# Kernel tuning notes

Measured on AMD Instinct MI355X. Metric: run time of the kernel, lower is better.

## Reference

```python
import jax, jax.numpy as jnp
import numpy as np


def setup_inputs() -> dict:
    key = jax.random.key(0)
    k1, k2 = jax.random.split(key)
    B, D, H, W = 32, 64, 32, 32
    K = 1024
    z_e = jax.random.normal(k1, (B, D, H, W), dtype=jnp.float32)
    # original init: uniform(-1/K, 1/K); use same scale
    emb = jax.random.uniform(k2, (K, D), dtype=jnp.float32, minval=-1.0 / K, maxval=1.0 / K)
    return {"z_e": z_e, "emb": emb}


COMMITMENT_COST = 0.25


def reference(z_e, emb):
    # z_e: [B, D, H, W], emb: [K, D]
    B, D, H, W = z_e.shape
    K = emb.shape[0]
    z = jnp.transpose(z_e, (0, 2, 3, 1))           # [B, H, W, D]
    flat = z.reshape(-1, D)                        # [N, D]
    N = flat.shape[0]

    dist = (
        jnp.sum(flat * flat, axis=1, keepdims=True)
        + jnp.sum(emb * emb, axis=1)
        - 2.0 * flat @ emb.T
    )
    idx = jnp.argmin(dist, axis=1)                 # [N]
    encodings = jax.nn.one_hot(idx, K, dtype=flat.dtype)  # [N, K]
    z_q = (encodings @ emb).reshape(z.shape)       # [B, H, W, D]

    e_latent_loss = jnp.mean((jax.lax.stop_gradient(z_q) - z) ** 2)
    q_latent_loss = jnp.mean((z_q - jax.lax.stop_gradient(z)) ** 2)
    loss = q_latent_loss + COMMITMENT_COST * e_latent_loss

    # straight-through estimator
    z_st = z + jax.lax.stop_gradient(z_q - z)

    avg_probs = jnp.sum(encodings, axis=0) / jnp.float32(N)
    perplexity = jnp.exp(-jnp.sum(avg_probs * jnp.log(avg_probs + 1e-10)))

    return (jnp.transpose(z_st, (0, 3, 1, 2)), loss, perplexity, encodings)
```

## Files before the change

kernel.cpp:

```cpp
#include <hip/hip_runtime.h>
#include <stdint.h>
#include <math.h>

constexpr int Kk  = 1024;

constexpr int OUT0_N   = 32 * 64 * 1024;
constexpr int OUT_LOSS = OUT0_N;
constexpr int OUT_PERP = OUT0_N + 1;
constexpr int OUT_ENC  = OUT0_N + 2;

constexpr size_t WS_CNT = 0;
constexpr size_t WS_LP  = 4096;
constexpr size_t WS_BN  = 12288;
constexpr size_t WS_MBN = 16384;
constexpr size_t WS_EBF = 20480;
constexpr size_t WS_KEY = 151552;

typedef short bf16x8 __attribute__((ext_vector_type(8)));
typedef float f32x16 __attribute__((ext_vector_type(16)));

__device__ __forceinline__ float norm64v(const float4* __restrict__ p) {
#pragma clang fp contract(off)
    float tt[64];
#pragma unroll
    for (int q = 0; q < 16; ++q) {
        float4 v = p[q];
        tt[4 * q + 0] = v.x * v.x;
        tt[4 * q + 1] = v.y * v.y;
        tt[4 * q + 2] = v.z * v.z;
        tt[4 * q + 3] = v.w * v.w;
    }
    float r[8];
#pragma unroll
    for (int j = 0; j < 8; ++j) r[j] = tt[j];
#pragma unroll
    for (int i = 8; i < 64; i += 8)
#pragma unroll
        for (int j = 0; j < 8; ++j) r[j] += tt[i + j];
    return ((r[0] + r[1]) + (r[2] + r[3])) + ((r[4] + r[5]) + (r[6] + r[7]));
}

__device__ __forceinline__ uint32_t fsort(float f) {
    uint32_t b = __float_as_uint(f);
    return (b & 0x80000000u) ? ~b : (b | 0x80000000u);
}

__device__ __forceinline__ unsigned short f2bf(float f) {
    uint32_t u = __float_as_uint(f);
    uint32_t r = (u + 0x7fffu + ((u >> 16) & 1u)) >> 16;
    return (unsigned short)r;
}

__device__ __forceinline__ unsigned long long
exact_key_bn(float A, const float* __restrict__ xr, const float* __restrict__ emb,
             const float* __restrict__ Bn_g, uint32_t code) {
    const float4* e4 = (const float4*)(emb + (size_t)code * 64);
    float4 ev[16];
#pragma unroll
    for (int q = 0; q < 16; ++q) ev[q] = e4[q];
    float C = 0.f;
#pragma unroll
    for (int q = 0; q < 16; ++q) {
        C = __builtin_fmaf(xr[4 * q + 0], ev[q].x, C);
        C = __builtin_fmaf(xr[4 * q + 1], ev[q].y, C);
        C = __builtin_fmaf(xr[4 * q + 2], ev[q].z, C);
        C = __builtin_fmaf(xr[4 * q + 3], ev[q].w, C);
    }
    float s = A + Bn_g[code];
    float dist = __builtin_fmaf(-2.f, C, s);
    return ((unsigned long long)fsort(dist) << 32) | code;
}

__global__ __launch_bounds__(256)
void norms_kernel(const float* __restrict__ emb, float* __restrict__ Bn_g,
                  float* __restrict__ maxbn, uint32_t* __restrict__ counts,
                  unsigned char* __restrict__ ebf16g) {
    __shared__ float wred[4];
    const int t = threadIdx.x, lane = t & 63, wv = t >> 6;
    const int code = blockIdx.x * 256 + t;
    float nn = norm64v((const float4*)(emb + (size_t)code * 64));
    Bn_g[code] = nn;
    if (blockIdx.x == 0) ((uint4*)counts)[t] = make_uint4(0u, 0u, 0u, 0u);

    {
        unsigned char* base = ebf16g + (size_t)(code >> 7) * 16384 + (size_t)(code & 127) * 128;
        const int swz = (code & 7) << 4;
        const float4* e4 = (const float4*)(emb + (size_t)code * 64);
#pragma unroll
        for (int q = 0; q < 16; ++q) {
            float4 v = e4[q];
            ushort4 bv;
            bv.x = f2bf(v.x); bv.y = f2bf(v.y); bv.z = f2bf(v.z); bv.w = f2bf(v.w);
            *(ushort4*)(base + ((q * 8) ^ swz)) = bv;
        }
    }
    float mx = nn;
#pragma unroll
    for (int m = 1; m < 64; m <<= 1) mx = fmaxf(mx, __shfl_xor(mx, m, 64));
    if (lane == 0) wred[wv] = mx;
    __syncthreads();
    if (t == 0)   maxbn[blockIdx.x * 2 + 0] = fmaxf(wred[0], wred[1]);
    if (t == 128) maxbn[blockIdx.x * 2 + 1] = fmaxf(wred[2], wred[3]);
}

__global__ __launch_bounds__(256, 5)
void dist_mfma(const float* __restrict__ z_e,
               const unsigned char* __restrict__ ebf16g,
               const float* __restrict__ Bn_g, const float* __restrict__ maxbn,
               unsigned long long* __restrict__ lockey, float* __restrict__ out) {
    __shared__ unsigned short ebf[128 * 64];
    __shared__ float Bn_s[128];
    const int t = threadIdx.x, lane = t & 63, wv = t >> 6, g = lane >> 5;
    const int rg = blockIdx.x >> 3, cg = blockIdx.x & 7;
    const int n0 = rg * 128, b = n0 >> 10, hw0 = n0 & 1023;
    const float* zb = z_e + (size_t)b * 65536 + hw0;

    {
        const float4* ep = (const float4*)(ebf16g + (size_t)cg * 16384);
#pragma unroll
        for (int it = 0; it < 4; ++it) {
            float4 v = ep[it * 256 + t];
            *(float4*)((char*)ebf + (size_t)(it * 256 + t) * 16) = v;
        }
    }
    if (t < 128) Bn_s[t] = Bn_g[cg * 128 + t];

    const int rowl = wv * 32 + (lane & 31);
    float xsq = 0.f;
    bf16x8 bfr[4];
#pragma unroll
    for (int s = 0; s < 4; ++s) {
        bf16x8 f;
#pragma unroll
        for (int e = 0; e < 8; ++e) {
            int d = s * 16 + g * 8 + e;
            float x = zb[(size_t)d * 1024 + rowl];
            xsq = __builtin_fmaf(x, x, xsq);
            f[e] = (short)f2bf(x);
        }
        bfr[s] = f;
    }
    xsq += __shfl_xor(xsq, 32, 64);
    const float margin = 0.017f * sqrtf(xsq * maxbn[cg]) + 1.0e-4f;
    __syncthreads();

    const int swz = (lane & 7) << 4;
    const char* ebase = (const char*)ebf + (lane & 31) * 128;

    float4* encz = (float4*)(out + OUT_ENC) + (size_t)blockIdx.x * 4096;
    const float4 zero4 = make_float4(0.f, 0.f, 0.f, 0.f);

    float runmin = 3.4e38f;
#pragma unroll 1
    for (int tm = 0; tm < 4; ++tm) {
        encz[(size_t)(tm * 2 + 0) * 256 + t] = zero4;
        encz[(size_t)(tm * 2 + 1) * 256 + t] = zero4;
        const char* p = ebase + tm * 4096;
        f32x16 acc = {};
#pragma unroll
        for (int s = 0; s < 4; ++s)
            acc = __builtin_amdgcn_mfma_f32_32x32x16_bf16(
                *(const bf16x8*)(p + ((s * 32 + g * 16) ^ swz)), bfr[s], acc, 0, 0, 0);
#pragma unroll
        for (int r = 0; r < 16; ++r) {
            int cl = tm * 32 + (r & 3) + 8 * (r >> 2) + 4 * g;
            runmin = fminf(runmin, __builtin_fmaf(-2.f, acc[r], Bn_s[cl]));
        }
    }
    runmin = fminf(runmin, __shfl_xor(runmin, 32, 64));
    const float thr = runmin + margin;

    uint32_t cnt = 0, c0 = 0, c1 = 0, c2 = 0;
#pragma unroll 1
    for (int tm = 0; tm < 4; ++tm) {
        encz[(size_t)(8 + tm * 2 + 0) * 256 + t] = zero4;
        encz[(size_t)(8 + tm * 2 + 1) * 256 + t] = zero4;
        const char* p = ebase + tm * 4096;
        f32x16 acc = {};
#pragma unroll
        for (int s = 0; s < 4; ++s)
            acc = __builtin_amdgcn_mfma_f32_32x32x16_bf16(
                *(const bf16x8*)(p + ((s * 32 + g * 16) ^ swz)), bfr[s], acc, 0, 0, 0);
#pragma unroll
        for (int r = 0; r < 16; ++r) {
            int cl = tm * 32 + (r & 3) + 8 * (r >> 2) + 4 * g;
            float sv = __builtin_fmaf(-2.f, acc[r], Bn_s[cl]);
            if (sv <= thr) {
                uint32_t gc = (uint32_t)(cg * 128 + cl);
                if (cnt == 0u) c0 = gc; else if (cnt == 1u) c1 = gc; else if (cnt == 2u) c2 = gc;
                ++cnt;
            }
        }
    }
    uint32_t pc = __shfl_xor(cnt, 32, 64);
    uint32_t p0 = __shfl_xor(c0, 32, 64);
    uint32_t p1 = __shfl_xor(c1, 32, 64);
    uint32_t p2 = __shfl_xor(c2, 32, 64);
    if (lane < 32) {
        uint32_t tot = cnt + pc;
        uint32_t lo;
        if (tot > 3u || tot == 0u) {
            lo = 3u << 30;
        } else {
            uint32_t a0 = c0, a1 = c1, a2 = c2;
            if (cnt == 0u)      { a0 = p0; a1 = p1; a2 = p2; }
            else if (cnt == 1u) { a1 = p0; a2 = p1; }
            else if (cnt == 2u) { a2 = p0; }
            if (tot < 2u) a1 = 0u;
            if (tot < 3u) a2 = 0u;
            lo = ((tot - 1u) << 30) | (a0 & 1023u) | ((a1 & 1023u) << 10) | ((a2 & 1023u) << 20);
        }
        unsigned long long key = ((unsigned long long)__float_as_uint(runmin) << 32) | lo;
        lockey[(size_t)(n0 + rowl) * 8 + cg] = key;
    }
}

__global__ __launch_bounds__(256)
void finish_kernel(const float* __restrict__ z_e, const float* __restrict__ emb,
                   const unsigned long long* __restrict__ lockey,
                   const float* __restrict__ Bn_g,
                   const float* __restrict__ maxbn,
                   uint32_t* __restrict__ counts, double* __restrict__ lp,
                   float* __restrict__ out) {
    __shared__ float zs[32 * 68];
    __shared__ float arow[32];
    __shared__ uint32_t scode[32];
    __shared__ uint8_t ncarr[32];
    __shared__ uint8_t ovfm[32];
    __shared__ uint8_t ovfnc[32];
    __shared__ unsigned long long pkey[32][6];
    __shared__ unsigned long long okey[32];
    __shared__ uint32_t pairbuf[192];
    __shared__ uint32_t ovfbuf[32];
    __shared__ uint32_t npairs, novf;
    __shared__ float mbg_s;
    __shared__ unsigned long long rbuf[4];
    __shared__ double lred[4];
    const int t = threadIdx.x, lane = t & 63, wv = t >> 6;
    const int n0 = blockIdx.x * 32;
    const int b = n0 >> 10, hw0 = n0 & 1023;
    const int hwi = t & 31, dg = t >> 5;
    const size_t base = (size_t)b * 65536 + (size_t)(dg * 8) * 1024 + hw0 + hwi;

    if (t == 0) {
        npairs = 0u; novf = 0u;
        float mb = maxbn[0];
#pragma unroll
        for (int i = 1; i < 8; ++i) mb = fmaxf(mb, maxbn[i]);
        mbg_s = mb;
    }

    float zreg[8];
#pragma unroll
    for (int k = 0; k < 8; ++k) zreg[k] = z_e[base + (size_t)k * 1024];
#pragma unroll
    for (int m = 0; m < 2; ++m)
        *(float4*)&zs[hwi * 68 + dg * 8 + 4 * m] =
            make_float4(zreg[4 * m], zreg[4 * m + 1], zreg[4 * m + 2], zreg[4 * m + 3]);
    __syncthreads();

    if (t < 32) {
        const unsigned long long* k8 = lockey + (size_t)(n0 + t) * 8;
        unsigned long long kws[8];
#pragma unroll
        for (int i = 0; i < 8; ++i) kws[i] = k8[i];
        float gmin = 3.4e38f;
#pragma unroll
        for (int i = 0; i < 8; ++i)
            gmin = fminf(gmin, __uint_as_float((uint32_t)(kws[i] >> 32)));
        float A = norm64v((const float4*)&zs[t * 68]);
        arow[t] = A;
        const float thr = gmin + 0.017f * sqrtf(A * mbg_s) + 1.0e-4f;

        int nc = 0; uint32_t cand[6]; uint32_t om = 0;
#pragma unroll
        for (int i = 0; i < 8; ++i) {
            float f = __uint_as_float((uint32_t)(kws[i] >> 32));
            if (f > thr) continue;
            uint32_t lo = (uint32_t)kws[i], cc = lo >> 30;
            if (cc == 3u) { om |= (1u << i); }
            else {
#pragma unroll
                for (uint32_t q = 0; q < 3u; ++q)
                    if (q <= cc) {
                        if (nc < 6) cand[nc] = (lo >> (10u * q)) & 1023u;
                        ++nc;
                    }
            }
        }
        if (nc > 6 || (nc == 0 && om == 0u)) {
            ncarr[t] = 255u;
            ovfbuf[atomicAdd(&novf, 1u)] = (uint32_t)t;
        } else if (om) {
            ncarr[t] = 0u;
            ovfm[t] = (uint8_t)om;
            ovfnc[t] = (uint8_t)nc;
            ovfbuf[atomicAdd(&novf, 1u)] = (uint32_t)t;
            if (nc > 0) {
                uint32_t bs = atomicAdd(&npairs, (uint32_t)nc);
#pragma unroll
                for (int q = 0; q < 6; ++q)
                    if (q < nc)
                        pairbuf[bs + q] = ((uint32_t)t << 13) | ((uint32_t)q << 10) | cand[q];
            }
        } else if (nc == 1) {
            ncarr[t] = 1u;
            scode[t] = cand[0];
        } else {
            ncarr[t] = (uint8_t)nc;
            uint32_t bs = atomicAdd(&npairs, (uint32_t)nc);
#pragma unroll
            for (int q = 0; q < 6; ++q)
                if (q < nc)
                    pairbuf[bs + q] = ((uint32_t)t << 13) | ((uint32_t)q << 10) | cand[q];
        }
    }
    __syncthreads();

    for (uint32_t p = t; p < npairs; p += 256u) {
        uint32_t pk = pairbuf[p];
        int row = (int)(pk >> 13), slot = (int)((pk >> 10) & 7u);
        pkey[row][slot] = exact_key_bn(arow[row], &zs[row * 68], emb, Bn_g, pk & 1023u);
    }
    __syncthreads();

    for (uint32_t o = 0; o < novf; ++o) {
        int row = (int)ovfbuf[o];
        const float* xr = &zs[row * 68];
        float A = arow[row];
        unsigned long long best = ~0ULL;
        if (ncarr[row] == 255u) {
#pragma unroll 1
            for (int cq = 0; cq < 4; ++cq) {
                unsigned long long key = exact_key_bn(A, xr, emb, Bn_g, (uint32_t)(t + cq * 256));
                best = (key < best) ? key : best;
            }
        } else {
            uint32_t om = ovfm[row];
#pragma unroll 1
            for (int i = 0; i < 8; ++i) {
                if ((om & (1u << i)) && t < 128) {
                    unsigned long long key = exact_key_bn(A, xr, emb, Bn_g, (uint32_t)(i * 128 + t));
                    best = (key < best) ? key : best;
                }
            }
        }
#pragma unroll
        for (int m = 1; m < 64; m <<= 1) {
            unsigned long long ok = __shfl_xor(best, m, 64);
            best = (ok < best) ? ok : best;
        }
        if (lane == 0) rbuf[wv] = best;
        __syncthreads();
        if (t == 0) {
            unsigned long long bb = rbuf[0];
#pragma unroll
            for (int w = 1; w < 4; ++w) bb = (rbuf[w] < bb) ? rbuf[w] : bb;
            if (ncarr[row] == 255u) scode[row] = (uint32_t)bb;
            else                    okey[row] = bb;
        }
        __syncthreads();
    }

    if (t < 32) {
        uint8_t k = ncarr[t];
        if (k == 0u) {
            unsigned long long bb = okey[t];
            int nc = (int)ovfnc[t];
#pragma unroll
            for (int q = 0; q < 6; ++q)
                if (q < nc && pkey[t][q] < bb) bb = pkey[t][q];
            scode[t] = (uint32_t)bb;
        } else if (k >= 2u && k != 255u) {
            unsigned long long bb = pkey[t][0];
#pragma unroll
            for (int q = 1; q < 6; ++q)
                if (q < (int)k && pkey[t][q] < bb) bb = pkey[t][q];
            scode[t] = (uint32_t)bb;
        }
    }
    __syncthreads();

    if (t < 32) {
        uint32_t code = scode[t];
        atomicAdd(&counts[code], 1u);
        out[(size_t)OUT_ENC + (size_t)(n0 + t) * 1024 + code] = 1.0f;
    }

    {
        const uint32_t code = scode[hwi];
        const float4* er4 = (const float4*)(emb + (size_t)code * 64) + dg * 2;
        double ls = 0.0;
#pragma unroll
        for (int k4 = 0; k4 < 2; ++k4) {
            float4 e4 = er4[k4];
            float f0 = e4.x, f1 = e4.y, f2 = e4.z, f3 = e4.w;
            size_t off = base + (size_t)(k4 * 4) * 1024;
            {
                float z = zreg[k4 * 4 + 0]; float tt = f0 - z;
                out[off] = z + tt;              ls += (double)tt * (double)tt;
            }
            {
                float z = zreg[k4 * 4 + 1]; float tt = f1 - z;
                out[off + 1024] = z + tt;       ls += (double)tt * (double)tt;
            }
            {
                float z = zreg[k4 * 4 + 2]; float tt = f2 - z;
                out[off + 2048] = z + tt;       ls += (double)tt * (double)tt;
            }
            {
                float z = zreg[k4 * 4 + 3]; float tt = f3 - z;
                out[off + 3072] = z + tt;       ls += (double)tt * (double)tt;
            }
        }
#pragma unroll
        for (int m = 32; m >= 1; m >>= 1) ls += __shfl_down(ls, m, 64);
        if ((t & 63) == 0) lred[t >> 6] = ls;
    }
    __syncthreads();
    if (t == 0) lp[blockIdx.x] = lred[0] + lred[1] + lred[2] + lred[3];
}

__global__ void scalar_kernel(const uint32_t* __restrict__ counts,
                              const double* __restrict__ lp,
                              float* __restrict__ out) {
    __shared__ double redl[4], redh[4];
    const int t = threadIdx.x;
    double ls = 0.0;
    for (int i = t; i < 1024; i += 256) ls += lp[i];
    double h = 0.0;
    for (int i = t; i < Kk; i += 256) {
        double p = (double)counts[i] * (1.0 / 32768.0);
        h += p * log(p + 1e-10);
    }
#pragma unroll
    for (int m = 32; m >= 1; m >>= 1) { ls += __shfl_down(ls, m, 64); h += __shfl_down(h, m, 64); }
    if ((t & 63) == 0) { redl[t >> 6] = ls; redh[t >> 6] = h; }
    __syncthreads();
    if (t == 0) {
        double L = redl[0] + redl[1] + redl[2] + redl[3];
        double H = redh[0] + redh[1] + redh[2] + redh[3];
        out[OUT_PERP] = (float)exp(-H);
        float m32 = (float)(L * (1.0 / 2097152.0));
        out[OUT_LOSS] = m32 + 0.25f * m32;
    }
}

extern "C" void kernel_launch(void* const* d_in, const int* in_sizes, int n_in,
                              void* d_out, int out_size, void* d_ws, size_t ws_size,
                              hipStream_t stream) {
    const float* z_e = (const float*)d_in[0];
    const float* emb = (const float*)d_in[1];
    float* out = (float*)d_out;
    char* ws = (char*)d_ws;

    uint32_t* counts = (uint32_t*)(ws + WS_CNT);
    double*   lp     = (double*)(ws + WS_LP);
    float*    Bn_g   = (float*)(ws + WS_BN);
    float*    mbn    = (float*)(ws + WS_MBN);
    unsigned char* ebf16g = (unsigned char*)(ws + WS_EBF);
    unsigned long long* lockey = (unsigned long long*)(ws + WS_KEY);

    norms_kernel<<<4, 256, 0, stream>>>(emb, Bn_g, mbn, counts, ebf16g);
    dist_mfma<<<2048, 256, 0, stream>>>(z_e, ebf16g, Bn_g, mbn, lockey, out);
    finish_kernel<<<1024, 256, 0, stream>>>(z_e, emb, lockey, Bn_g, mbn, counts, lp, out);
    scalar_kernel<<<1, 256, 0, stream>>>(counts, lp, out);
}
```

Baseline: 202.2 us.

## Widen dist tiles to 256 codes and convert embeddings to bf16 in-kernel

Each distance block now covers 256 codebook entries instead of 128. That halves the grid to 1024 blocks and halves the per-row partial keys the finish kernel has to merge (4 instead of 8). The global bf16 pre-converted codebook is dropped: each block loads fp32 embeddings and converts and swizzles them into LDS itself. This removes a workspace round trip but repeats the conversion work in every block. The one-hot zeroing is changed to write rows contiguously, and the larger LDS tile lowers the occupancy bound from 5 to 4 blocks per CU.

```diff
diff --git a/kernel.cpp b/kernel.cpp
--- a/kernel.cpp
+++ b/kernel.cpp
@@ -13,8 +13,7 @@
 constexpr size_t WS_LP  = 4096;
 constexpr size_t WS_BN  = 12288;
 constexpr size_t WS_MBN = 16384;
-constexpr size_t WS_EBF = 20480;
-constexpr size_t WS_KEY = 151552;
+constexpr size_t WS_KEY = 16400;
 
 typedef short bf16x8 __attribute__((ext_vector_type(8)));
 typedef float f32x16 __attribute__((ext_vector_type(16)));
@@ -73,57 +72,46 @@
 
 __global__ __launch_bounds__(256)
 void norms_kernel(const float* __restrict__ emb, float* __restrict__ Bn_g,
-                  float* __restrict__ maxbn, uint32_t* __restrict__ counts,
-                  unsigned char* __restrict__ ebf16g) {
+                  float* __restrict__ maxbn, uint32_t* __restrict__ counts) {
     __shared__ float wred[4];
     const int t = threadIdx.x, lane = t & 63, wv = t >> 6;
     const int code = blockIdx.x * 256 + t;
     float nn = norm64v((const float4*)(emb + (size_t)code * 64));
     Bn_g[code] = nn;
     if (blockIdx.x == 0) ((uint4*)counts)[t] = make_uint4(0u, 0u, 0u, 0u);
+    float mx = nn;
+#pragma unroll
+    for (int m = 1; m < 64; m <<= 1) mx = fmaxf(mx, __shfl_xor(mx, m, 64));
+    if (lane == 0) wred[wv] = mx;
+    __syncthreads();
+    if (t == 0)
+        maxbn[blockIdx.x] = fmaxf(fmaxf(wred[0], wred[1]), fmaxf(wred[2], wred[3]));
+}
+
+__global__ __launch_bounds__(256, 4)
+void dist_mfma(const float* __restrict__ z_e, const float* __restrict__ emb,
+               const float* __restrict__ Bn_g, const float* __restrict__ maxbn,
+               unsigned long long* __restrict__ lockey, float* __restrict__ out) {
+    __shared__ unsigned short ebf[256 * 64];
+    __shared__ float Bn_s[256];
+    const int t = threadIdx.x, lane = t & 63, wv = t >> 6, g = lane >> 5;
+    const int rg = blockIdx.x >> 2, cg = blockIdx.x & 3;
+    const int n0 = rg * 128, b = n0 >> 10, hw0 = n0 & 1023;
+    const float* zb = z_e + (size_t)b * 65536 + hw0;
 
     {
-        unsigned char* base = ebf16g + (size_t)(code >> 7) * 16384 + (size_t)(code & 127) * 128;
-        const int swz = (code & 7) << 4;
-        const float4* e4 = (const float4*)(emb + (size_t)code * 64);
-#pragma unroll
-        for (int q = 0; q < 16; ++q) {
-            float4 v = e4[q];
+        const float4* ep = (const float4*)(emb + (size_t)cg * 16384);
+#pragma unroll
+        for (int it = 0; it < 16; ++it) {
+            int j = t + it * 256;
+            float4 v = ep[j];
+            int code = j >> 4, q = j & 15;
             ushort4 bv;
             bv.x = f2bf(v.x); bv.y = f2bf(v.y); bv.z = f2bf(v.z); bv.w = f2bf(v.w);
-            *(ushort4*)(base + ((q * 8) ^ swz)) = bv;
-        }
-    }
-    float mx = nn;
-#pragma unroll
-    for (int m = 1; m < 64; m <<= 1) mx = fmaxf(mx, __shfl_xor(mx, m, 64));
-    if (lane == 0) wred[wv] = mx;
-    __syncthreads();
-    if (t == 0)   maxbn[blockIdx.x * 2 + 0] = fmaxf(wred[0], wred[1]);
-    if (t == 128) maxbn[blockIdx.x * 2 + 1] = fmaxf(wred[2], wred[3]);
-}
-
-__global__ __launch_bounds__(256, 5)
-void dist_mfma(const float* __restrict__ z_e,
-               const unsigned char* __restrict__ ebf16g,
-               const float* __restrict__ Bn_g, const float* __restrict__ maxbn,
-               unsigned long long* __restrict__ lockey, float* __restrict__ out) {
-    __shared__ unsigned short ebf[128 * 64];
-    __shared__ float Bn_s[128];
-    const int t = threadIdx.x, lane = t & 63, wv = t >> 6, g = lane >> 5;
-    const int rg = blockIdx.x >> 3, cg = blockIdx.x & 7;
-    const int n0 = rg * 128, b = n0 >> 10, hw0 = n0 & 1023;
-    const float* zb = z_e + (size_t)b * 65536 + hw0;
-
-    {
-        const float4* ep = (const float4*)(ebf16g + (size_t)cg * 16384);
-#pragma unroll
-        for (int it = 0; it < 4; ++it) {
-            float4 v = ep[it * 256 + t];
-            *(float4*)((char*)ebf + (size_t)(it * 256 + t) * 16) = v;
-        }
-    }
-    if (t < 128) Bn_s[t] = Bn_g[cg * 128 + t];
+            *(ushort4*)((char*)ebf + code * 128 + ((q * 8) ^ ((code & 7) << 4))) = bv;
+        }
+    }
+    Bn_s[t] = Bn_g[cg * 256 + t];
 
     const int rowl = wv * 32 + (lane & 31);
     float xsq = 0.f;
@@ -147,14 +135,19 @@
     const int swz = (lane & 7) << 4;
     const char* ebase = (const char*)ebf + (lane & 31) * 128;
 
-    float4* encz = (float4*)(out + OUT_ENC) + (size_t)blockIdx.x * 4096;
+    float* encp = out + OUT_ENC;
     const float4 zero4 = make_float4(0.f, 0.f, 0.f, 0.f);
+    const int erow0 = t >> 6;
+    const int ec4 = t & 63;
 
     float runmin = 3.4e38f;
 #pragma unroll 1
-    for (int tm = 0; tm < 4; ++tm) {
-        encz[(size_t)(tm * 2 + 0) * 256 + t] = zero4;
-        encz[(size_t)(tm * 2 + 1) * 256 + t] = zero4;
+    for (int tm = 0; tm < 8; ++tm) {
+#pragma unroll
+        for (int u = 0; u < 2; ++u) {
+            int row = (tm * 2 + u) * 4 + erow0;
+            ((float4*)(encp + (size_t)(n0 + row) * 1024 + cg * 256))[ec4] = zero4;
+        }
         const char* p = ebase + tm * 4096;
         f32x16 acc = {};
 #pragma unroll
@@ -172,9 +165,12 @@
 
     uint32_t cnt = 0, c0 = 0, c1 = 0, c2 = 0;
 #pragma unroll 1
-    for (int tm = 0; tm < 4; ++tm) {
-        encz[(size_t)(8 + tm * 2 + 0) * 256 + t] = zero4;
-        encz[(size_t)(8 + tm * 2 + 1) * 256 + t] = zero4;
+    for (int tm = 0; tm < 8; ++tm) {
+#pragma unroll
+        for (int u = 0; u < 2; ++u) {
+            int row = 64 + (tm * 2 + u) * 4 + erow0;
+            ((float4*)(encp + (size_t)(n0 + row) * 1024 + cg * 256))[ec4] = zero4;
+        }
         const char* p = ebase + tm * 4096;
         f32x16 acc = {};
 #pragma unroll
@@ -186,7 +182,7 @@
             int cl = tm * 32 + (r & 3) + 8 * (r >> 2) + 4 * g;
             float sv = __builtin_fmaf(-2.f, acc[r], Bn_s[cl]);
             if (sv <= thr) {
-                uint32_t gc = (uint32_t)(cg * 128 + cl);
+                uint32_t gc = (uint32_t)(cg * 256 + cl);
                 if (cnt == 0u) c0 = gc; else if (cnt == 1u) c1 = gc; else if (cnt == 2u) c2 = gc;
                 ++cnt;
             }
@@ -211,7 +207,7 @@
             lo = ((tot - 1u) << 30) | (a0 & 1023u) | ((a1 & 1023u) << 10) | ((a2 & 1023u) << 20);
         }
         unsigned long long key = ((unsigned long long)__float_as_uint(runmin) << 32) | lo;
-        lockey[(size_t)(n0 + rowl) * 8 + cg] = key;
+        lockey[(size_t)(n0 + rowl) * 4 + cg] = key;
     }
 }
 
@@ -244,9 +240,7 @@
 
     if (t == 0) {
         npairs = 0u; novf = 0u;
-        float mb = maxbn[0];
-#pragma unroll
-        for (int i = 1; i < 8; ++i) mb = fmaxf(mb, maxbn[i]);
+        float mb = fmaxf(fmaxf(maxbn[0], maxbn[1]), fmaxf(maxbn[2], maxbn[3]));
         mbg_s = mb;
     }
 
@@ -260,13 +254,13 @@
     __syncthreads();
 
     if (t < 32) {
-        const unsigned long long* k8 = lockey + (size_t)(n0 + t) * 8;
-        unsigned long long kws[8];
-#pragma unroll
-        for (int i = 0; i < 8; ++i) kws[i] = k8[i];
+        const unsigned long long* k4 = lockey + (size_t)(n0 + t) * 4;
+        unsigned long long kws[4];
+#pragma unroll
+        for (int i = 0; i < 4; ++i) kws[i] = k4[i];
         float gmin = 3.4e38f;
 #pragma unroll
-        for (int i = 0; i < 8; ++i)
+        for (int i = 0; i < 4; ++i)
             gmin = fminf(gmin, __uint_as_float((uint32_t)(kws[i] >> 32)));
         float A = norm64v((const float4*)&zs[t * 68]);
         arow[t] = A;
@@ -274,7 +268,7 @@
 
         int nc = 0; uint32_t cand[6]; uint32_t om = 0;
 #pragma unroll
-        for (int i = 0; i < 8; ++i) {
+        for (int i = 0; i < 4; ++i) {
             float f = __uint_as_float((uint32_t)(kws[i] >> 32));
             if (f > thr) continue;
             uint32_t lo = (uint32_t)kws[i], cc = lo >> 30;
@@ -338,9 +332,9 @@
         } else {
             uint32_t om = ovfm[row];
 #pragma unroll 1
-            for (int i = 0; i < 8; ++i) {
-                if ((om & (1u << i)) && t < 128) {
-                    unsigned long long key = exact_key_bn(A, xr, emb, Bn_g, (uint32_t)(i * 128 + t));
+            for (int i = 0; i < 4; ++i) {
+                if (om & (1u << i)) {
+                    unsigned long long key = exact_key_bn(A, xr, emb, Bn_g, (uint32_t)(i * 256 + t));
                     best = (key < best) ? key : best;
                 }
             }
@@ -458,11 +452,10 @@
     double*   lp     = (double*)(ws + WS_LP);
     float*    Bn_g   = (float*)(ws + WS_BN);
     float*    mbn    = (float*)(ws + WS_MBN);
-    unsigned char* ebf16g = (unsigned char*)(ws + WS_EBF);
     unsigned long long* lockey = (unsigned long long*)(ws + WS_KEY);
 
-    norms_kernel<<<4, 256, 0, stream>>>(emb, Bn_g, mbn, counts, ebf16g);
-    dist_mfma<<<2048, 256, 0, stream>>>(z_e, ebf16g, Bn_g, mbn, lockey, out);
+    norms_kernel<<<4, 256, 0, stream>>>(emb, Bn_g, mbn, counts);
+    dist_mfma<<<1024, 256, 0, stream>>>(z_e, emb, Bn_g, mbn, lockey, out);
     finish_kernel<<<1024, 256, 0, stream>>>(z_e, emb, lockey, Bn_g, mbn, counts, lp, out);
     scalar_kernel<<<1, 256, 0, stream>>>(counts, lp, out);
 }
```

Result: faster. 195.9 us (-3.1%).
